# Optimization experiments

Hardware: AMD Instinct MI355X
Metric: run time of the kernel (lower is better)

Reference implementation:

```python
import math
import jax, jax.numpy as jnp
import numpy as np

B, S, E, A, H, L, V = 4, 1024, 1024, 64, 16, 2, 32000
EPS = 1e-5
SCALE = math.sqrt(E)  # torch code scales by sqrt(input_dim) = sqrt(embedding_dim)
W_INIT_SCALE = 0.05   # torch.rand is U[0,1); scaled down for numerically sane softmax


def setup_inputs() -> dict:
    key = jax.random.key(0)
    ks = jax.random.split(key, 6)
    return {
        "x": jax.random.randint(ks[0], (B, S), 0, V),
        "emb": jax.random.normal(ks[1], (V, E), dtype=jnp.float32) * 0.02,
        "ln_gamma": jnp.ones((L, E), dtype=jnp.float32),
        "ln_beta": jnp.zeros((L, E), dtype=jnp.float32),
        "Wq": jax.random.uniform(ks[2], (L, H, A, E), dtype=jnp.float32) * W_INIT_SCALE,
        "Wk": jax.random.uniform(ks[3], (L, H, A, E), dtype=jnp.float32) * W_INIT_SCALE,
        "Wv": jax.random.uniform(ks[4], (L, H, E, E), dtype=jnp.float32) * W_INIT_SCALE,
    }


def _attn_layer(h, gamma, beta, wq, wk, wv):
    # h: [B,H,S,E]; LayerNorm over last dim (biased variance, like torch)
    mu = jnp.mean(h, axis=-1, keepdims=True)
    var = jnp.mean(jnp.square(h - mu), axis=-1, keepdims=True)
    hn = (h - mu) * jax.lax.rsqrt(var + EPS) * gamma + beta
    q = jnp.einsum('bhse,hae->bhsa', hn, wq)   # [B,H,S,A]
    k = jnp.einsum('bhse,hae->bhsa', hn, wk)   # [B,H,S,A]
    v = jnp.einsum('bhse,hoe->bhso', hn, wv)   # [B,H,S,E]
    scores = jnp.einsum('bhsa,bhta->bhst', q, k) / SCALE  # [B,H,S,S]
    w = jax.nn.softmax(scores, axis=-1)
    return jnp.einsum('bhst,bhto->bhso', w, v)  # [B,H,S,E]


def reference(x, emb, ln_gamma, ln_beta, Wq, Wk, Wv):
    # embed then replicate across heads: [B,S,E] -> [B,H,S,E]
    h = jnp.broadcast_to(emb[x][:, None, :, :], (B, H, S, E))
    for l in range(L):
        h = _attn_layer(h, ln_gamma[l], ln_beta[l], Wq[l], Wk[l], Wv[l])
    return h
```

## Files before the change

### kernel.cpp

```cpp
#include <hip/hip_runtime.h>

#define B_ 4
#define S_ 1024
#define E_ 1024
#define A_ 64
#define H_ 16
#define L_ 2

static constexpr float LN_EPS = 1e-5f;
static constexpr float INV_SCALE = 1.0f / 32.0f;

typedef __attribute__((ext_vector_type(8))) short bf16x8;
typedef __attribute__((ext_vector_type(4))) float f32x4;

__device__ __forceinline__ unsigned short f2bf(float f) {
  unsigned u = __float_as_uint(f);
  u += 0x7fffu + ((u >> 16) & 1u);
  return (unsigned short)(u >> 16);
}
__device__ __forceinline__ float bf2f(unsigned short s) {
  return __uint_as_float(((unsigned)s) << 16);
}

__device__ __forceinline__ float block_sum256(float v, float* red) {
#pragma unroll
  for (int o = 32; o > 0; o >>= 1) v += __shfl_down(v, o, 64);
  const int lane = threadIdx.x & 63;
  const int w = threadIdx.x >> 6;
  if (lane == 0) red[w] = v;
  __syncthreads();
  if (threadIdx.x == 0) red[0] = red[0] + red[1] + red[2] + red[3];
  __syncthreads();
  float r = red[0];
  __syncthreads();
  return r;
}

__device__ __forceinline__ float block_max256(float v, float* red) {
#pragma unroll
  for (int o = 32; o > 0; o >>= 1) v = fmaxf(v, __shfl_down(v, o, 64));
  const int lane = threadIdx.x & 63;
  const int w = threadIdx.x >> 6;
  if (lane == 0) red[w] = v;
  __syncthreads();
  if (threadIdx.x == 0) red[0] = fmaxf(fmaxf(red[0], red[1]), fmaxf(red[2], red[3]));
  __syncthreads();
  float r = red[0];
  __syncthreads();
  return r;
}

__global__ __launch_bounds__(256) void cvt_f32_bf16(const float* __restrict__ in,
                                                    unsigned short* __restrict__ out, long n) {
  long i = ((long)blockIdx.x * 256 + threadIdx.x) * 4;
  const long stride = (long)gridDim.x * 1024;
  for (; i < n; i += stride) {
    float4 v = *(const float4*)(in + i);
    ushort4 o;
    o.x = f2bf(v.x); o.y = f2bf(v.y); o.z = f2bf(v.z); o.w = f2bf(v.w);
    *(ushort4*)(out + i) = o;
  }
}

__global__ __launch_bounds__(256) void embed_ln_kernel(
    const int* __restrict__ x, const float* __restrict__ emb,
    const float* __restrict__ gamma, const float* __restrict__ beta,
    unsigned short* __restrict__ out) {
  __shared__ float red[4];
  const int row = blockIdx.x;
  const int tid = threadIdx.x;
  const float* src = emb + (long)x[row] * E_;
  float4 v = *(const float4*)(src + tid * 4);
  const float mean = block_sum256(v.x + v.y + v.z + v.w, red) * (1.f / E_);
  float dx = v.x - mean, dy = v.y - mean, dz = v.z - mean, dw = v.w - mean;
  const float var = block_sum256(dx * dx + dy * dy + dz * dz + dw * dw, red) * (1.f / E_);
  const float rstd = rsqrtf(var + LN_EPS);
  float4 g = *(const float4*)(gamma + tid * 4);
  float4 b = *(const float4*)(beta + tid * 4);
  ushort4 o;
  o.x = f2bf(dx * rstd * g.x + b.x);
  o.y = f2bf(dy * rstd * g.y + b.y);
  o.z = f2bf(dz * rstd * g.z + b.z);
  o.w = f2bf(dw * rstd * g.w + b.w);
  *(ushort4*)(out + (long)row * E_ + tid * 4) = o;
}

__global__ __launch_bounds__(256) void ln_f32_bf16_kernel(
    const float* __restrict__ h, const float* __restrict__ gamma,
    const float* __restrict__ beta, unsigned short* __restrict__ out) {
  __shared__ float red[4];
  const long row = blockIdx.x;
  const int tid = threadIdx.x;
  float4 v = *(const float4*)(h + row * (long)E_ + tid * 4);
  const float mean = block_sum256(v.x + v.y + v.z + v.w, red) * (1.f / E_);
  float dx = v.x - mean, dy = v.y - mean, dz = v.z - mean, dw = v.w - mean;
  const float var = block_sum256(dx * dx + dy * dy + dz * dz + dw * dw, red) * (1.f / E_);
  const float rstd = rsqrtf(var + LN_EPS);
  float4 g = *(const float4*)(gamma + tid * 4);
  float4 b = *(const float4*)(beta + tid * 4);
  ushort4 o;
  o.x = f2bf(dx * rstd * g.x + b.x);
  o.y = f2bf(dy * rstd * g.y + b.y);
  o.z = f2bf(dz * rstd * g.z + b.z);
  o.w = f2bf(dw * rstd * g.w + b.w);
  *(ushort4*)(out + row * E_ + tid * 4) = o;
}

__global__ __launch_bounds__(256) void softmax_bf16_kernel(unsigned short* __restrict__ sc) {
  __shared__ float red[4];
  unsigned short* p = sc + (long)blockIdx.x * S_;
  const int tid = threadIdx.x;
  ushort4 raw = *(const ushort4*)(p + tid * 4);
  float v0 = bf2f(raw.x), v1 = bf2f(raw.y), v2 = bf2f(raw.z), v3 = bf2f(raw.w);
  float m = block_max256(fmaxf(fmaxf(v0, v1), fmaxf(v2, v3)), red);
  v0 = __expf(v0 - m); v1 = __expf(v1 - m); v2 = __expf(v2 - m); v3 = __expf(v3 - m);
  const float s = block_sum256(v0 + v1 + v2 + v3, red);
  const float inv = 1.f / s;
  ushort4 o;
  o.x = f2bf(v0 * inv); o.y = f2bf(v1 * inv); o.z = f2bf(v2 * inv); o.w = f2bf(v3 * inv);
  *(ushort4*)(p + tid * 4) = o;
}

__device__ __forceinline__ void gload_lds16(const void* g, void* l) {
  __builtin_amdgcn_global_load_lds((const __attribute__((address_space(1))) void*)g,
                                   (__attribute__((address_space(3))) void*)l, 16, 0, 0);
}

template <int ROWS>
__device__ __forceinline__ void stage_tile(const unsigned short* __restrict__ src, int ldK,
                                           unsigned short* lds, int tid) {
  const int rb = tid >> 3;
  const int gslot = (tid & 7) ^ (rb & 7);
  const int wbase = (tid >> 6) * 512;
#pragma unroll
  for (int i = 0; i < ROWS / 32; ++i) {
    const unsigned short* g = src + (long)(i * 32 + rb) * ldK + gslot * 8;
    gload_lds16(g, lds + i * 2048 + wbase);
  }
}

__device__ __forceinline__ bf16x8 lds_frag(const unsigned short* base, int r, int slot) {
  const int byteoff = (r << 7) + ((slot ^ (r & 7)) << 4);
  return *(const bf16x8*)((const char*)base + byteoff);
}

template <int BM, int BN, bool OUT_BF16>
__global__ __launch_bounds__(256) void mfma_gemm_nt(
    const unsigned short* __restrict__ Aall, const unsigned short* __restrict__ Ball,
    void* __restrict__ Call, int M, int N, int K,
    long aSB, long aSH, long bSB, long bSH, int Hn, float alpha) {
  __shared__ unsigned short As[BM * 64];
  __shared__ unsigned short Bs[BN * 64];
  const int batch = blockIdx.z;
  const int bb = batch / Hn, hh = batch % Hn;
  const unsigned short* Ap = Aall + (long)bb * aSB + (long)hh * aSH;
  const unsigned short* Bp = Ball + (long)bb * bSB + (long)hh * bSH;
  const int tid = threadIdx.x;
  const int lane = tid & 63;
  const int wave = tid >> 6;
  const int wr = wave >> 1, wc = wave & 1;
  const int bm = blockIdx.x * BM, bn = blockIdx.y * BN;
  constexpr int FM = BM / 32, FN = BN / 32;

  f32x4 acc[FM][FN];
#pragma unroll
  for (int i = 0; i < FM; ++i)
#pragma unroll
    for (int j = 0; j < FN; ++j) acc[i][j] = (f32x4)(0.f);

  for (int k0 = 0; k0 < K; k0 += 64) {
    stage_tile<BM>(Ap + (long)bm * K + k0, K, As, tid);
    stage_tile<BN>(Bp + (long)bn * K + k0, K, Bs, tid);
    __syncthreads();
#pragma unroll
    for (int kb = 0; kb < 2; ++kb) {
      const int slot = (kb << 2) + (lane >> 4);
      bf16x8 af[FM], bfv[FN];
#pragma unroll
      for (int mi = 0; mi < FM; ++mi)
        af[mi] = lds_frag(As, wr * (BM / 2) + mi * 16 + (lane & 15), slot);
#pragma unroll
      for (int ni = 0; ni < FN; ++ni)
        bfv[ni] = lds_frag(Bs, wc * (BN / 2) + ni * 16 + (lane & 15), slot);
#pragma unroll
      for (int mi = 0; mi < FM; ++mi)
#pragma unroll
        for (int ni = 0; ni < FN; ++ni)
          acc[mi][ni] = __builtin_amdgcn_mfma_f32_16x16x32_bf16(af[mi], bfv[ni], acc[mi][ni], 0, 0, 0);
    }
    __syncthreads();
  }

#pragma unroll
  for (int mi = 0; mi < FM; ++mi) {
    const int row = bm + wr * (BM / 2) + mi * 16 + ((lane >> 4) << 2);
#pragma unroll
    for (int ni = 0; ni < FN; ++ni) {
      const int col = bn + wc * (BN / 2) + ni * 16 + (lane & 15);
#pragma unroll
      for (int r = 0; r < 4; ++r) {
        const float v = acc[mi][ni][r] * alpha;
        const long idx = (long)batch * M * N + (long)(row + r) * N + col;
        if constexpr (OUT_BF16)
          ((unsigned short*)Call)[idx] = f2bf(v);
        else
          ((float*)Call)[idx] = v;
      }
    }
  }
}

extern "C" void kernel_launch(void* const* d_in, const int* in_sizes, int n_in,
                              void* d_out, int out_size, void* d_ws, size_t ws_size,
                              hipStream_t stream) {
  const int* x = (const int*)d_in[0];
  const float* emb = (const float*)d_in[1];
  const float* gamma = (const float*)d_in[2];
  const float* beta = (const float*)d_in[3];
  const float* Wq = (const float*)d_in[4];
  const float* Wk = (const float*)d_in[5];
  const float* Wv = (const float*)d_in[6];
  float* out = (float*)d_out;

  const long WQK_N = (long)L_ * H_ * A_ * E_;
  const long WV_N = (long)L_ * H_ * E_ * E_;
  const long HN_N = (long)B_ * H_ * S_ * E_;
  const long QK_N = (long)B_ * H_ * S_ * A_;
  unsigned short* wq_bf = (unsigned short*)d_ws;
  unsigned short* wk_bf = wq_bf + WQK_N;
  unsigned short* wv_bf = wk_bf + WQK_N;
  unsigned short* hn = wv_bf + WV_N;
  unsigned short* q = hn + HN_N;
  unsigned short* k = q + QK_N;
  unsigned short* v_t = k + QK_N;
  unsigned short* sc = v_t + HN_N;

  const dim3 blk(256);
  cvt_f32_bf16<<<512, blk, 0, stream>>>(Wq, wq_bf, WQK_N);
  cvt_f32_bf16<<<512, blk, 0, stream>>>(Wk, wk_bf, WQK_N);
  cvt_f32_bf16<<<2048, blk, 0, stream>>>(Wv, wv_bf, WV_N);

  for (int l = 0; l < L_; ++l) {
    long hSB, hSH;
    if (l == 0) {
      embed_ln_kernel<<<B_ * S_, blk, 0, stream>>>(x, emb, gamma, beta, hn);
      hSB = (long)S_ * E_; hSH = 0;
    } else {
      ln_f32_bf16_kernel<<<B_ * H_ * S_, blk, 0, stream>>>(
          out, gamma + (long)l * E_, beta + (long)l * E_, hn);
      hSB = (long)H_ * S_ * E_; hSH = (long)S_ * E_;
    }
    mfma_gemm_nt<128, 64, true><<<dim3(8, 1, 64), blk, 0, stream>>>(
        hn, wq_bf + l * H_ * A_ * E_, q, S_, A_, E_,
        hSB, hSH, 0L, (long)A_ * E_, H_, 1.f);
    mfma_gemm_nt<128, 64, true><<<dim3(8, 1, 64), blk, 0, stream>>>(
        hn, wk_bf + l * H_ * A_ * E_, k, S_, A_, E_,
        hSB, hSH, 0L, (long)A_ * E_, H_, 1.f);
    mfma_gemm_nt<128, 128, true><<<dim3(8, 8, 64), blk, 0, stream>>>(
        wv_bf + (long)l * H_ * E_ * E_, hn, v_t, E_, S_, E_,
        0L, (long)E_ * E_, hSB, hSH, H_, 1.f);
    mfma_gemm_nt<128, 128, true><<<dim3(8, 8, 64), blk, 0, stream>>>(
        q, k, sc, S_, S_, A_,
        (long)H_ * S_ * A_, (long)S_ * A_, (long)H_ * S_ * A_, (long)S_ * A_, H_, INV_SCALE);
    softmax_bf16_kernel<<<B_ * H_ * S_, blk, 0, stream>>>(sc);
    mfma_gemm_nt<128, 128, false><<<dim3(8, 8, 64), blk, 0, stream>>>(
        sc, v_t, out, S_, E_, S_,
        (long)H_ * S_ * S_, (long)S_ * S_, (long)H_ * E_ * S_, (long)E_ * S_, H_, 1.f);
  }
}
```

Measured before the change: 1.194 ms.

## Add 256x256 double-buffered GEMM, fuse Q/K projection, store layer-0 output in bf16

Adds a new 512-thread GEMM kernel with 256x256 tiles, 128KB of dynamic LDS double buffering, an XCD-aware workgroup remap and setprio around the MFMA blocks. It is used for the large V projection and the attention-times-V GEMMs to raise data reuse and overlap loads with compute. Wq and Wk are concatenated so one GEMM produces Q and K together. The layer-0 hidden output is written as bf16 into the output buffer and read back by a bf16 LayerNorm, which halves that round-trip traffic at some precision cost. The larger tiles use more registers and LDS per block, which limits occupancy.

```diff
diff --git a/kernel.cpp b/kernel.cpp
--- a/kernel.cpp
+++ b/kernel.cpp
@@ -56,6 +56,25 @@
   const long stride = (long)gridDim.x * 1024;
   for (; i < n; i += stride) {
     float4 v = *(const float4*)(in + i);
+    ushort4 o;
+    o.x = f2bf(v.x); o.y = f2bf(v.y); o.z = f2bf(v.z); o.w = f2bf(v.w);
+    *(ushort4*)(out + i) = o;
+  }
+}
+
+__global__ __launch_bounds__(256) void cvt_qk_concat(const float* __restrict__ Wq,
+                                                     const float* __restrict__ Wk,
+                                                     unsigned short* __restrict__ out) {
+  const long total = (long)L_ * H_ * 128 * E_;
+  long i = ((long)blockIdx.x * 256 + threadIdx.x) * 4;
+  const long stride = (long)gridDim.x * 1024;
+  for (; i < total; i += stride) {
+    const long e = i % E_;
+    const long rowhe = i / E_;
+    const int row = (int)(rowhe % 128);
+    const long lh = rowhe / 128;
+    const float* src = (row < 64 ? Wq : Wk) + (lh * 64 + (row & 63)) * E_ + e;
+    float4 v = *(const float4*)src;
     ushort4 o;
     o.x = f2bf(v.x); o.y = f2bf(v.y); o.z = f2bf(v.z); o.w = f2bf(v.w);
     *(ushort4*)(out + i) = o;
@@ -85,15 +104,16 @@
   *(ushort4*)(out + (long)row * E_ + tid * 4) = o;
 }
 
-__global__ __launch_bounds__(256) void ln_f32_bf16_kernel(
-    const float* __restrict__ h, const float* __restrict__ gamma,
+__global__ __launch_bounds__(256) void ln_bf16_kernel(
+    const unsigned short* __restrict__ h, const float* __restrict__ gamma,
     const float* __restrict__ beta, unsigned short* __restrict__ out) {
   __shared__ float red[4];
   const long row = blockIdx.x;
   const int tid = threadIdx.x;
-  float4 v = *(const float4*)(h + row * (long)E_ + tid * 4);
-  const float mean = block_sum256(v.x + v.y + v.z + v.w, red) * (1.f / E_);
-  float dx = v.x - mean, dy = v.y - mean, dz = v.z - mean, dw = v.w - mean;
+  ushort4 raw = *(const ushort4*)(h + row * (long)E_ + tid * 4);
+  float vx = bf2f(raw.x), vy = bf2f(raw.y), vz = bf2f(raw.z), vw = bf2f(raw.w);
+  const float mean = block_sum256(vx + vy + vz + vw, red) * (1.f / E_);
+  float dx = vx - mean, dy = vy - mean, dz = vz - mean, dw = vw - mean;
   const float var = block_sum256(dx * dx + dy * dy + dz * dz + dw * dw, red) * (1.f / E_);
   const float rstd = rsqrtf(var + LN_EPS);
   float4 g = *(const float4*)(gamma + tid * 4);
@@ -127,14 +147,14 @@
 }
 
 template <int ROWS>
-__device__ __forceinline__ void stage_tile(const unsigned short* __restrict__ src, int ldK,
+__device__ __forceinline__ void stage_tile(const unsigned short* __restrict__ src, int ldRow,
                                            unsigned short* lds, int tid) {
   const int rb = tid >> 3;
   const int gslot = (tid & 7) ^ (rb & 7);
   const int wbase = (tid >> 6) * 512;
 #pragma unroll
   for (int i = 0; i < ROWS / 32; ++i) {
-    const unsigned short* g = src + (long)(i * 32 + rb) * ldK + gslot * 8;
+    const unsigned short* g = src + (long)(i * 32 + rb) * ldRow + gslot * 8;
     gload_lds16(g, lds + i * 2048 + wbase);
   }
 }
@@ -147,7 +167,7 @@
 template <int BM, int BN, bool OUT_BF16>
 __global__ __launch_bounds__(256) void mfma_gemm_nt(
     const unsigned short* __restrict__ Aall, const unsigned short* __restrict__ Ball,
-    void* __restrict__ Call, int M, int N, int K,
+    void* __restrict__ Call, int M, int N, int K, int lda, int ldb,
     long aSB, long aSH, long bSB, long bSH, int Hn, float alpha) {
   __shared__ unsigned short As[BM * 64];
   __shared__ unsigned short Bs[BN * 64];
@@ -169,8 +189,8 @@
     for (int j = 0; j < FN; ++j) acc[i][j] = (f32x4)(0.f);
 
   for (int k0 = 0; k0 < K; k0 += 64) {
-    stage_tile<BM>(Ap + (long)bm * K + k0, K, As, tid);
-    stage_tile<BN>(Bp + (long)bn * K + k0, K, Bs, tid);
+    stage_tile<BM>(Ap + (long)bm * lda + k0, lda, As, tid);
+    stage_tile<BN>(Bp + (long)bn * ldb + k0, ldb, Bs, tid);
     __syncthreads();
 #pragma unroll
     for (int kb = 0; kb < 2; ++kb) {
@@ -201,6 +221,107 @@
       for (int r = 0; r < 4; ++r) {
         const float v = acc[mi][ni][r] * alpha;
         const long idx = (long)batch * M * N + (long)(row + r) * N + col;
+        if constexpr (OUT_BF16)
+          ((unsigned short*)Call)[idx] = f2bf(v);
+        else
+          ((float*)Call)[idx] = v;
+      }
+    }
+  }
+}
+
+__device__ __forceinline__ void stage_unit256(const unsigned short* __restrict__ src, int ldRow,
+                                              char* lds_unit, int tid) {
+#pragma unroll
+  for (int i = 0; i < 2; ++i) {
+    const int r = i * 128 + (tid >> 2);
+    const int sg = (tid & 3) ^ ((r >> 1) & 3);
+    const unsigned short* g = src + (long)r * ldRow + sg * 8;
+    gload_lds16(g, lds_unit + i * 8192 + ((tid >> 6) << 10));
+  }
+}
+
+__device__ __forceinline__ bf16x8 lds_frag256(const char* opbase, int kh, int r, int ss) {
+  return *(const bf16x8*)(opbase + kh * 16384 + r * 64 + ((ss ^ ((r >> 1) & 3)) << 4));
+}
+
+template <bool OUT_BF16>
+__global__ __launch_bounds__(512, 2) void mfma_gemm256_nt(
+    const unsigned short* __restrict__ Aall, const unsigned short* __restrict__ Ball,
+    void* __restrict__ Call, int M, int N, int K, int lda, int ldb,
+    long aSB, long aSH, long bSB, long bSH, int Hn, float alpha) {
+  extern __shared__ char lds[];
+  const int nx = gridDim.x, ny = gridDim.y;
+  const int nwg = nx * ny * gridDim.z;
+  int f = blockIdx.x + nx * (blockIdx.y + ny * blockIdx.z);
+  if ((nwg & 7) == 0) f = (f & 7) * (nwg >> 3) + (f >> 3);
+  const int bx = f % nx;
+  const int by = (f / nx) % ny;
+  const int batch = f / (nx * ny);
+
+  const int bb = batch / Hn, hh = batch % Hn;
+  const unsigned short* Ap = Aall + (long)bb * aSB + (long)hh * aSH + (long)bx * 256 * lda;
+  const unsigned short* Bp = Ball + (long)bb * bSB + (long)hh * bSH + (long)by * 256 * ldb;
+  const int tid = threadIdx.x;
+  const int lane = tid & 63;
+  const int w = tid >> 6;
+  const int wr = w >> 2, wc = w & 3;
+
+  f32x4 acc[8][4];
+#pragma unroll
+  for (int i = 0; i < 8; ++i)
+#pragma unroll
+    for (int j = 0; j < 4; ++j) acc[i][j] = (f32x4)(0.f);
+
+  const int NT = K >> 6;
+  stage_unit256(Ap, lda, lds, tid);
+  stage_unit256(Bp, ldb, lds + 32768, tid);
+  stage_unit256(Ap + 32, lda, lds + 16384, tid);
+  stage_unit256(Bp + 32, ldb, lds + 32768 + 16384, tid);
+  asm volatile("s_waitcnt vmcnt(0)\n\ts_barrier" ::: "memory");
+
+  for (int t = 0; t < NT; ++t) {
+    const char* cur = lds + (t & 1) * 65536;
+    char* nxt = lds + ((t + 1) & 1) * 65536;
+    const unsigned short* An = Ap + (long)(t + 1) * 64;
+    const unsigned short* Bn = Bp + (long)(t + 1) * 64;
+    const bool pf = (t + 1 < NT);
+#pragma unroll
+    for (int kh = 0; kh < 2; ++kh) {
+      bf16x8 a[8], b[4];
+      const int ss = lane >> 4;
+#pragma unroll
+      for (int mi = 0; mi < 8; ++mi)
+        a[mi] = lds_frag256(cur, kh, wr * 128 + mi * 16 + (lane & 15), ss);
+#pragma unroll
+      for (int ni = 0; ni < 4; ++ni)
+        b[ni] = lds_frag256(cur + 32768, kh, wc * 64 + ni * 16 + (lane & 15), ss);
+      if (pf) {
+        stage_unit256(An + kh * 32, lda, nxt + kh * 16384, tid);
+        stage_unit256(Bn + kh * 32, ldb, nxt + 32768 + kh * 16384, tid);
+      }
+      asm volatile("s_barrier" ::: "memory");
+      __builtin_amdgcn_s_setprio(1);
+#pragma unroll
+      for (int mi = 0; mi < 8; ++mi)
+#pragma unroll
+        for (int ni = 0; ni < 4; ++ni)
+          acc[mi][ni] = __builtin_amdgcn_mfma_f32_16x16x32_bf16(a[mi], b[ni], acc[mi][ni], 0, 0, 0);
+      __builtin_amdgcn_s_setprio(0);
+      asm volatile("s_waitcnt vmcnt(4)\n\ts_barrier" ::: "memory");
+    }
+  }
+
+#pragma unroll
+  for (int mi = 0; mi < 8; ++mi) {
+    const int row0 = bx * 256 + wr * 128 + mi * 16 + ((lane >> 4) << 2);
+#pragma unroll
+    for (int ni = 0; ni < 4; ++ni) {
+      const int col = by * 256 + wc * 64 + ni * 16 + (lane & 15);
+#pragma unroll
+      for (int r = 0; r < 4; ++r) {
+        const float v = acc[mi][ni][r] * alpha;
+        const long idx = (long)batch * M * N + (long)(row0 + r) * N + col;
         if constexpr (OUT_BF16)
           ((unsigned short*)Call)[idx] = f2bf(v);
         else
@@ -222,23 +343,27 @@
   const float* Wv = (const float*)d_in[6];
   float* out = (float*)d_out;
 
-  const long WQK_N = (long)L_ * H_ * A_ * E_;
+  (void)hipFuncSetAttribute(reinterpret_cast<const void*>(&mfma_gemm256_nt<true>),
+                            hipFuncAttributeMaxDynamicSharedMemorySize, 131072);
+  (void)hipFuncSetAttribute(reinterpret_cast<const void*>(&mfma_gemm256_nt<false>),
+                            hipFuncAttributeMaxDynamicSharedMemorySize, 131072);
+
+  const long WQK_N = (long)L_ * H_ * 128 * E_;
   const long WV_N = (long)L_ * H_ * E_ * E_;
   const long HN_N = (long)B_ * H_ * S_ * E_;
-  const long QK_N = (long)B_ * H_ * S_ * A_;
-  unsigned short* wq_bf = (unsigned short*)d_ws;
-  unsigned short* wk_bf = wq_bf + WQK_N;
-  unsigned short* wv_bf = wk_bf + WQK_N;
+  const long QK_N = (long)B_ * H_ * S_ * 128;
+  unsigned short* wqk = (unsigned short*)d_ws;
+  unsigned short* wv_bf = wqk + WQK_N;
   unsigned short* hn = wv_bf + WV_N;
-  unsigned short* q = hn + HN_N;
-  unsigned short* k = q + QK_N;
-  unsigned short* v_t = k + QK_N;
+  unsigned short* qk = hn + HN_N;
+  unsigned short* v_t = qk + QK_N;
   unsigned short* sc = v_t + HN_N;
-
-  const dim3 blk(256);
-  cvt_f32_bf16<<<512, blk, 0, stream>>>(Wq, wq_bf, WQK_N);
-  cvt_f32_bf16<<<512, blk, 0, stream>>>(Wk, wk_bf, WQK_N);
-  cvt_f32_bf16<<<2048, blk, 0, stream>>>(Wv, wv_bf, WV_N);
+  unsigned short* hid0 = (unsigned short*)d_out;
+
+  const dim3 blk(256), blk512(512);
+  const dim3 grid256(4, 4, 64);
+  cvt_qk_concat<<<2048, blk, 0, stream>>>(Wq, Wk, wqk);
+  cvt_f32_bf16<<<4096, blk, 0, stream>>>(Wv, wv_bf, WV_N);
 
   for (int l = 0; l < L_; ++l) {
     long hSB, hSH;
@@ -246,25 +371,28 @@
       embed_ln_kernel<<<B_ * S_, blk, 0, stream>>>(x, emb, gamma, beta, hn);
       hSB = (long)S_ * E_; hSH = 0;
     } else {
-      ln_f32_bf16_kernel<<<B_ * H_ * S_, blk, 0, stream>>>(
-          out, gamma + (long)l * E_, beta + (long)l * E_, hn);
+      ln_bf16_kernel<<<B_ * H_ * S_, blk, 0, stream>>>(
+          hid0, gamma + (long)l * E_, beta + (long)l * E_, hn);
       hSB = (long)H_ * S_ * E_; hSH = (long)S_ * E_;
     }
-    mfma_gemm_nt<128, 64, true><<<dim3(8, 1, 64), blk, 0, stream>>>(
-        hn, wq_bf + l * H_ * A_ * E_, q, S_, A_, E_,
-        hSB, hSH, 0L, (long)A_ * E_, H_, 1.f);
-    mfma_gemm_nt<128, 64, true><<<dim3(8, 1, 64), blk, 0, stream>>>(
-        hn, wk_bf + l * H_ * A_ * E_, k, S_, A_, E_,
-        hSB, hSH, 0L, (long)A_ * E_, H_, 1.f);
-    mfma_gemm_nt<128, 128, true><<<dim3(8, 8, 64), blk, 0, stream>>>(
-        wv_bf + (long)l * H_ * E_ * E_, hn, v_t, E_, S_, E_,
+    mfma_gemm_nt<128, 128, true><<<dim3(8, 1, 64), blk, 0, stream>>>(
+        hn, wqk + (long)l * H_ * 128 * E_, qk, S_, 128, E_, E_, E_,
+        hSB, hSH, 0L, (long)128 * E_, H_, 1.f);
+    mfma_gemm256_nt<true><<<grid256, blk512, 131072, stream>>>(
+        wv_bf + (long)l * H_ * E_ * E_, hn, v_t, E_, S_, E_, E_, E_,
         0L, (long)E_ * E_, hSB, hSH, H_, 1.f);
     mfma_gemm_nt<128, 128, true><<<dim3(8, 8, 64), blk, 0, stream>>>(
-        q, k, sc, S_, S_, A_,
-        (long)H_ * S_ * A_, (long)S_ * A_, (long)H_ * S_ * A_, (long)S_ * A_, H_, INV_SCALE);
+        qk, qk + 64, sc, S_, S_, 64, 128, 128,
+        (long)H_ * S_ * 128, (long)S_ * 128, (long)H_ * S_ * 128, (long)S_ * 128, H_, INV_SCALE);
     softmax_bf16_kernel<<<B_ * H_ * S_, blk, 0, stream>>>(sc);
-    mfma_gemm_nt<128, 128, false><<<dim3(8, 8, 64), blk, 0, stream>>>(
-        sc, v_t, out, S_, E_, S_,
-        (long)H_ * S_ * S_, (long)S_ * S_, (long)H_ * E_ * S_, (long)E_ * S_, H_, 1.f);
-  }
-}
+    if (l == 0) {
+      mfma_gemm256_nt<true><<<grid256, blk512, 131072, stream>>>(
+          sc, v_t, hid0, S_, E_, S_, S_, S_,
+          (long)H_ * S_ * S_, (long)S_ * S_, (long)H_ * E_ * S_, (long)E_ * S_, H_, 1.f);
+    } else {
+      mfma_gemm256_nt<false><<<grid256, blk512, 131072, stream>>>(
+          sc, v_t, out, S_, E_, S_, S_, S_,
+          (long)H_ * S_ * S_, (long)S_ * S_, (long)H_ * E_ * S_, (long)E_ * S_, H_, 1.f);
+    }
+  }
+}
```

Result: faster. 1.017 ms (-14.8%).
